# Kernel optimization log

Measured on AMD Instinct MI355X. Metric: run time of the kernel, lower is better.

Reference implementation:

```python
import jax, jax.numpy as jnp
import numpy as np

N_HEAD = 16
HEAD_DIM = 64
R_VALUE = 256
EPS_LN = 1e-5


def _orf(x, omega, b):
    # orthogonal random features: sqrt(2/r) * cos(x @ omega.T + b)
    r = b.shape[0]
    return jnp.sqrt(2.0 / r) * jnp.cos(x @ omega.T + b)


def _layernorm(x, gamma, beta):
    m = jnp.mean(x, axis=-1, keepdims=True)
    v = jnp.var(x, axis=-1, keepdims=True)
    return (x - m) / jnp.sqrt(v + EPS_LN) * gamma + beta


def setup_inputs() -> dict:
    key = jax.random.key(0)
    ks = jax.random.split(key, 12)
    B, L = 4, 2048
    dm = N_HEAD * HEAD_DIM  # 1024
    inp = {}
    inp["pre_query"] = jax.random.normal(ks[0], (B, L, dm), jnp.float32)
    inp["pre_key"] = jax.random.normal(ks[1], (B, L, dm), jnp.float32)
    inp["pre_value"] = jax.random.normal(ks[2], (B, L, dm), jnp.float32)
    inp["wq"] = jax.random.normal(ks[3], (dm, dm), jnp.float32) * 0.02
    inp["wk"] = jax.random.normal(ks[4], (dm, dm), jnp.float32) * 0.02
    inp["wv"] = jax.random.normal(ks[5], (dm, dm), jnp.float32) * 0.02
    inp["wo"] = jax.random.normal(ks[6], (dm, dm), jnp.float32) * 0.02
    inp["gamma"] = jnp.ones((dm,), jnp.float32)
    inp["beta"] = jnp.zeros((dm,), jnp.float32)
    G = jax.random.normal(ks[7], (R_VALUE, HEAD_DIM), jnp.float32)
    omega, _ = jnp.linalg.qr(G)  # (r, head_dim), orthonormal columns
    inp["omega"] = omega
    inp["b"] = jax.random.uniform(ks[8], (R_VALUE,), jnp.float32) * 2.0 * jnp.pi
    return inp


def reference(pre_query, pre_key, pre_value, wq, wk, wv, wo, gamma, beta, omega, b):
    B, L, dm = pre_query.shape
    H, D = N_HEAD, dm // N_HEAD
    q = (pre_query @ wq.T).reshape(B, L, H, D)
    k = (pre_key @ wk.T).reshape(B, L, H, D)
    v = (pre_value @ wv.T).reshape(B, L, H, D)

    qp = _orf(q, omega, b)  # (B,L,H,R)
    kp = _orf(k, omega, b)  # (B,L,H,R)

    # causal Performer attention as a linear-attention recurrence:
    # S_t = S_{t-1} + k'_t v_t^T ; z_t = z_{t-1} + k'_t
    # out_t = (q'_t . S_t) / clamp(q'_t . z_t)
    R = b.shape[0]
    S0 = jnp.zeros((B, H, R, D), qp.dtype)
    z0 = jnp.zeros((B, H, R), qp.dtype)

    def step(carry, xs):
        S, z = carry
        q_t, k_t, v_t = xs  # (B,H,R),(B,H,R),(B,H,D)
        S = S + k_t[..., :, None] * v_t[..., None, :]
        z = z + k_t
        num = jnp.einsum('bhr,bhrd->bhd', q_t, S)
        den = jnp.clip(jnp.einsum('bhr,bhr->bh', q_t, z), 1e-6, None)
        return (S, z), num / (den[..., None] + 1e-6)

    xs = (qp.transpose(1, 0, 2, 3), kp.transpose(1, 0, 2, 3), v.transpose(1, 0, 2, 3))
    _, out = jax.lax.scan(step, (S0, z0), xs)  # (L,B,H,D)
    out = out.transpose(1, 0, 2, 3).reshape(B, L, dm)

    pre_result = out @ wo.T
    return _layernorm(pre_result + pre_query, gamma, beta)
```

## Files before the change

kernel.cpp:

```cpp
#include <hip/hip_runtime.h>
#include <hip/hip_bf16.h>


typedef float f4 __attribute__((ext_vector_type(4)));
typedef __attribute__((ext_vector_type(8))) short bf16x8;
typedef __attribute__((ext_vector_type(4))) float f32x4;
typedef unsigned short u16x4 __attribute__((ext_vector_type(4)));
typedef unsigned short u16x8 __attribute__((ext_vector_type(8)));

#define B_  4
#define L_  2048
#define H_  16
#define D_  64
#define DM_ 1024
#define R_  256
#define C_  64
#define NC_ (L_ / C_)
#define M_  (B_ * L_)
#define M2_ (M_ * H_)

static __device__ __forceinline__ unsigned short f2bu(float x) {
    __hip_bfloat16 h = __float2bfloat16(x);
    return *(unsigned short*)&h;
}
static __device__ __forceinline__ float bu2f(unsigned short u) {
    union { unsigned int i; float f; } c; c.i = ((unsigned int)u) << 16; return c.f;
}

typedef __attribute__((address_space(3))) void lds_void_t;
typedef __attribute__((address_space(1))) const void gvoid_t;
static __device__ __forceinline__ void gload16(const void* g, void* l) {
    __builtin_amdgcn_global_load_lds((gvoid_t*)g, (lds_void_t*)l, 16, 0, 0);
}

__launch_bounds__(256)
__global__ void cvt_bf16(const float* __restrict__ in, unsigned short* __restrict__ out, int n4) {
    int i = blockIdx.x * 256 + threadIdx.x;
    if (i < n4) {
        f4 v = *(const f4*)&in[(size_t)i * 4];
        ushort4 o;
        o.x = f2bu(v[0]); o.y = f2bu(v[1]); o.z = f2bu(v[2]); o.w = f2bu(v[3]);
        *(ushort4*)&out[(size_t)i * 4] = o;
    }
}

__launch_bounds__(256)
__global__ void cvt_bf16_x3(const float* __restrict__ i0, const float* __restrict__ i1,
                            const float* __restrict__ i2,
                            unsigned short* __restrict__ o0, unsigned short* __restrict__ o1,
                            unsigned short* __restrict__ o2, int n4) {
    const int z = blockIdx.z;
    const float* in = (z == 0) ? i0 : (z == 1) ? i1 : i2;
    unsigned short* out = (z == 0) ? o0 : (z == 1) ? o1 : o2;
    int i = blockIdx.x * 256 + threadIdx.x;
    if (i < n4) {
        f4 v = *(const f4*)&in[(size_t)i * 4];
        ushort4 o;
        o.x = f2bu(v[0]); o.y = f2bu(v[1]); o.z = f2bu(v[2]); o.w = f2bu(v[3]);
        *(ushort4*)&out[(size_t)i * 4] = o;
    }
}

__launch_bounds__(256)
__global__ void gemm_mfma_b3(const unsigned short* __restrict__ A0, const unsigned short* __restrict__ A1,
                             const unsigned short* __restrict__ A2,
                             const unsigned short* __restrict__ B0, const unsigned short* __restrict__ B1,
                             const unsigned short* __restrict__ B2,
                             unsigned short* __restrict__ C0, unsigned short* __restrict__ C1,
                             unsigned short* __restrict__ C2,
                             int M, int N, int K) {
    __shared__ unsigned short Asl[3][128 * 32];
    __shared__ unsigned short Bsl[3][128 * 32];
    const int z = blockIdx.z;
    const unsigned short* A  = (z == 0) ? A0 : (z == 1) ? A1 : A2;
    const unsigned short* Bw = (z == 0) ? B0 : (z == 1) ? B1 : B2;
    unsigned short*       Cb = (z == 0) ? C0 : (z == 1) ? C1 : C2;
    const int t = threadIdx.x;
    const int lane = t & 63, w = t >> 6;
    const int wr = w >> 1, wc = w & 1;
    const int nwg = gridDim.x * gridDim.y;
    const int bid = blockIdx.y * gridDim.x + blockIdx.x;
    const int cpx = nwg >> 3;
    const int swz = (bid & 7) * cpx + (bid >> 3);
    const int row0 = (swz / gridDim.x) * 128, col0 = (swz % gridDim.x) * 128;
    const int sr0 = t >> 2;
    const int ssw = (((t & 3) ^ ((t >> 3) & 3)) * 8);
    const int lg = lane >> 4, lr = lane & 15;
    const int aslot = (lg ^ ((lr >> 1) & 3)) * 8;

#define STAGE_B3(buf, kkk) do { \
        gload16(&A [(size_t)(row0 + sr0)      * K + (kkk) + ssw], &Asl[buf][t * 8]); \
        gload16(&A [(size_t)(row0 + sr0 + 64) * K + (kkk) + ssw], &Asl[buf][(t + 256) * 8]); \
        gload16(&Bw[(size_t)(col0 + sr0)      * K + (kkk) + ssw], &Bsl[buf][t * 8]); \
        gload16(&Bw[(size_t)(col0 + sr0 + 64) * K + (kkk) + ssw], &Bsl[buf][(t + 256) * 8]); \
    } while (0)
#define COMPUTE_B3(buf) do { \
        bf16x8 af[4], bfr[4]; \
        _Pragma("unroll") \
        for (int m = 0; m < 4; ++m) \
            af[m] = *(const bf16x8*)&Asl[buf][(wr * 64 + m * 16 + lr) * 32 + aslot]; \
        _Pragma("unroll") \
        for (int n = 0; n < 4; ++n) \
            bfr[n] = *(const bf16x8*)&Bsl[buf][(wc * 64 + n * 16 + lr) * 32 + aslot]; \
        _Pragma("unroll") \
        for (int m = 0; m < 4; ++m) \
            _Pragma("unroll") \
            for (int n = 0; n < 4; ++n) \
                acc[m][n] = __builtin_amdgcn_mfma_f32_16x16x32_bf16(af[m], bfr[n], acc[m][n], 0, 0, 0); \
    } while (0)

    f32x4 acc[4][4] = {};
    STAGE_B3(0, 0);
    STAGE_B3(1, 32);
    int cur = 0;
    for (int kk = 0; kk + 64 < K; kk += 32) {
        int nx = cur + 2; if (nx >= 3) nx -= 3;
        STAGE_B3(nx, kk + 64);
        asm volatile("s_waitcnt vmcnt(8)" ::: "memory");
        __builtin_amdgcn_sched_barrier(0);
        __builtin_amdgcn_s_barrier();
        COMPUTE_B3(cur);
        __builtin_amdgcn_s_barrier();
        cur = (cur == 2) ? 0 : cur + 1;
    }
    asm volatile("s_waitcnt vmcnt(4)" ::: "memory");
    __builtin_amdgcn_sched_barrier(0);
    __builtin_amdgcn_s_barrier();
    COMPUTE_B3(cur);
    __builtin_amdgcn_s_barrier();
    cur = (cur == 2) ? 0 : cur + 1;
    asm volatile("s_waitcnt vmcnt(0)" ::: "memory");
    __builtin_amdgcn_sched_barrier(0);
    __builtin_amdgcn_s_barrier();
    COMPUTE_B3(cur);
#undef STAGE_B3
#undef COMPUTE_B3
#pragma unroll
    for (int m = 0; m < 4; ++m)
#pragma unroll
        for (int n = 0; n < 4; ++n)
#pragma unroll
            for (int i = 0; i < 4; ++i) {
                int r  = row0 + wr * 64 + m * 16 + lg * 4 + i;
                int cc = col0 + wc * 64 + n * 16 + lr;
                Cb[(size_t)r * N + cc] = f2bu(acc[m][n][i]);
            }
}

__launch_bounds__(256)
__global__ void gemm_out(const unsigned short* __restrict__ A,
                         const unsigned short* __restrict__ Bw,
                         const float* __restrict__ resid,
                         float* __restrict__ Cf,
                         int M, int N, int K) {
    __shared__ unsigned short Asl[3][64 * 32];
    __shared__ unsigned short Bsl[3][128 * 32];
    const int t = threadIdx.x;
    const int lane = t & 63, w = t >> 6;
    const int nwg = gridDim.x * gridDim.y;
    const int bid = blockIdx.y * gridDim.x + blockIdx.x;
    const int cpx = nwg >> 3;
    const int swz = (bid & 7) * cpx + (bid >> 3);
    const int row0 = (swz / gridDim.x) * 64, col0 = (swz % gridDim.x) * 128;
    const int sr0 = t >> 2;
    const int ssw = (((t & 3) ^ ((t >> 3) & 3)) * 8);
    const int lg = lane >> 4, lr = lane & 15;
    const int aslot = (lg ^ ((lr >> 1) & 3)) * 8;

#define STAGE_O(buf, kkk) do { \
        gload16(&A [(size_t)(row0 + sr0)      * K + (kkk) + ssw], &Asl[buf][t * 8]); \
        gload16(&Bw[(size_t)(col0 + sr0)      * K + (kkk) + ssw], &Bsl[buf][t * 8]); \
        gload16(&Bw[(size_t)(col0 + sr0 + 64) * K + (kkk) + ssw], &Bsl[buf][(t + 256) * 8]); \
    } while (0)
#define COMPUTE_O(buf) do { \
        bf16x8 af[4], bfr[2]; \
        _Pragma("unroll") \
        for (int m = 0; m < 4; ++m) \
            af[m] = *(const bf16x8*)&Asl[buf][(m * 16 + lr) * 32 + aslot]; \
        _Pragma("unroll") \
        for (int n = 0; n < 2; ++n) \
            bfr[n] = *(const bf16x8*)&Bsl[buf][(w * 32 + n * 16 + lr) * 32 + aslot]; \
        _Pragma("unroll") \
        for (int m = 0; m < 4; ++m) \
            _Pragma("unroll") \
            for (int n = 0; n < 2; ++n) \
                acc[m][n] = __builtin_amdgcn_mfma_f32_16x16x32_bf16(af[m], bfr[n], acc[m][n], 0, 0, 0); \
    } while (0)

    f32x4 acc[4][2] = {};
    STAGE_O(0, 0);
    STAGE_O(1, 32);
    int cur = 0;
    for (int kk = 0; kk + 64 < K; kk += 32) {
        int nx = cur + 2; if (nx >= 3) nx -= 3;
        STAGE_O(nx, kk + 64);
        asm volatile("s_waitcnt vmcnt(6)" ::: "memory");
        __builtin_amdgcn_sched_barrier(0);
        __builtin_amdgcn_s_barrier();
        COMPUTE_O(cur);
        __builtin_amdgcn_s_barrier();
        cur = (cur == 2) ? 0 : cur + 1;
    }
    asm volatile("s_waitcnt vmcnt(3)" ::: "memory");
    __builtin_amdgcn_sched_barrier(0);
    __builtin_amdgcn_s_barrier();
    COMPUTE_O(cur);
    __builtin_amdgcn_s_barrier();
    cur = (cur == 2) ? 0 : cur + 1;
    asm volatile("s_waitcnt vmcnt(0)" ::: "memory");
    __builtin_amdgcn_sched_barrier(0);
    __builtin_amdgcn_s_barrier();
    COMPUTE_O(cur);
#undef STAGE_O
#undef COMPUTE_O
#pragma unroll
    for (int m = 0; m < 4; ++m)
#pragma unroll
        for (int n = 0; n < 2; ++n)
#pragma unroll
            for (int i = 0; i < 4; ++i) {
                int r  = row0 + m * 16 + lg * 4 + i;
                int cc = col0 + w * 32 + n * 16 + lr;
                size_t off = (size_t)r * N + cc;
                Cf[off] = acc[m][n][i] + resid[off];
            }
}

#define RS_STRIDE 272
__launch_bounds__(256)
__global__ void feat_mfma_b2(const unsigned short* __restrict__ X0, const unsigned short* __restrict__ X1,
                             const unsigned short* __restrict__ om,
                             const float* __restrict__ bvec,
                             unsigned short* __restrict__ O0, unsigned short* __restrict__ O1) {
    __shared__ unsigned short Xs[2 * 64 * 32];
    __shared__ unsigned short Pool[64 * RS_STRIDE];
    const int z = blockIdx.z;
    const unsigned short* X = z ? X1 : X0;
    unsigned short* out = z ? O1 : O0;
    const int t = threadIdx.x;
    const int lane = t & 63, w = t >> 6;
    const int lg = lane >> 4, lr = lane & 15;
    const int m0 = blockIdx.x * 64;
    const int aslot = (lg ^ ((lr >> 1) & 3)) * 8;

#pragma unroll
    for (int i = 0; i < 2; ++i) {
        int cch = i * 256 + t;
        int ks = cch >> 8, row = (cch >> 2) & 63;
        int sub = ((cch & 3) ^ ((cch >> 3) & 3)) * 8;
        gload16(&X[(size_t)(m0 + row) * 64 + ks * 32 + sub], &Xs[cch * 8]);
    }
#pragma unroll
    for (int i = 0; i < 8; ++i) {
        int cch = i * 256 + t;
        int ks = cch >> 10, r = (cch >> 2) & 255;
        int sub = ((cch & 3) ^ ((cch >> 3) & 3)) * 8;
        gload16(&om[(size_t)r * 64 + ks * 32 + sub], &Pool[cch * 8]);
    }
    __syncthreads();

    f32x4 acc[4][4] = {};
#pragma unroll
    for (int ks = 0; ks < 2; ++ks) {
        bf16x8 af[4], bfr[4];
#pragma unroll
        for (int m = 0; m < 4; ++m)
            af[m] = *(const bf16x8*)&Xs[ks * 2048 + (m * 16 + lr) * 32 + aslot];
#pragma unroll
        for (int n = 0; n < 4; ++n)
            bfr[n] = *(const bf16x8*)&Pool[ks * 8192 + (w * 64 + n * 16 + lr) * 32 + aslot];
#pragma unroll
        for (int m = 0; m < 4; ++m)
#pragma unroll
            for (int n = 0; n < 4; ++n)
                acc[m][n] = __builtin_amdgcn_mfma_f32_16x16x32_bf16(af[m], bfr[n], acc[m][n], 0, 0, 0);
    }
    __syncthreads();

    const float scale = 0.08838834764831845f;
#pragma unroll
    for (int n = 0; n < 4; ++n) {
        const int col = w * 64 + n * 16 + lr;
        const float bb = bvec[col];
#pragma unroll
        for (int m = 0; m < 4; ++m)
#pragma unroll
            for (int ii = 0; ii < 4; ++ii)
                Pool[(m * 16 + lg * 4 + ii) * RS_STRIDE + col] = f2bu(scale * __cosf(acc[m][n][ii] + bb));
    }
    __syncthreads();
#pragma unroll
    for (int i = 0; i < 8; ++i) {
        int cch = i * 256 + t;
        int row = cch >> 5, colc = (cch & 31) * 8;
        u16x8 vv = *(const u16x8*)&Pool[row * RS_STRIDE + colc];
        *(u16x8*)&out[(size_t)(m0 + row) * 256 + colc] = vv;
    }
}

__launch_bounds__(256)
__global__ void passA_mfma(const unsigned short* __restrict__ kp, const unsigned short* __restrict__ vb,
                           unsigned short* __restrict__ kvT, float* __restrict__ ksum) {
    __shared__ __align__(16) unsigned short KPt[256][72];
    __shared__ __align__(16) unsigned short Vt[64][72];
    const int c = blockIdx.x, h = blockIdx.y, bz = blockIdx.z;
    const int t = threadIdx.x;
    const int lane = t & 63, w = t >> 6;
    const int lg = lane >> 4, lr = lane & 15;
    const int l0 = c * C_;
    const int bh = bz * H_ + h;

    {
        const int l4 = (t & 15) * 4, rs = (t >> 4) * 16;
        u16x8 row[4][2];
#pragma unroll
        for (int i = 0; i < 4; ++i) {
            const unsigned short* src = &kp[((size_t)(bz * L_ + l0 + l4 + i) * H_ + h) * R_ + rs];
            row[i][0] = *(const u16x8*)src;
            row[i][1] = *(const u16x8*)(src + 8);
        }
#pragma unroll
        for (int q = 0; q < 16; ++q) {
            u16x4 pk = { row[0][q >> 3][q & 7], row[1][q >> 3][q & 7],
                         row[2][q >> 3][q & 7], row[3][q >> 3][q & 7] };
            *(u16x4*)&KPt[rs + q][l4] = pk;
        }
    }
    {
        const int d4 = (t & 15) * 4, ls = (t >> 4) * 4;
        u16x4 x[4];
#pragma unroll
        for (int i = 0; i < 4; ++i)
            x[i] = *(const u16x4*)&vb[(size_t)(bz * L_ + l0 + ls + i) * DM_ + h * 64 + d4];
#pragma unroll
        for (int q = 0; q < 4; ++q) {
            u16x4 pk = { x[0][q], x[1][q], x[2][q], x[3][q] };
            *(u16x4*)&Vt[d4 + q][ls] = pk;
        }
    }
    __syncthreads();

    f32x4 acc[4][4] = {};
#pragma unroll
    for (int ks = 0; ks < 2; ++ks) {
        bf16x8 af[4], bfr[4];
#pragma unroll
        for (int m = 0; m < 4; ++m)
            af[m] = *(const bf16x8*)&KPt[64 * w + 16 * m + lr][ks * 32 + lg * 8];
#pragma unroll
        for (int n = 0; n < 4; ++n)
            bfr[n] = *(const bf16x8*)&Vt[16 * n + lr][ks * 32 + lg * 8];
#pragma unroll
        for (int m = 0; m < 4; ++m)
#pragma unroll
            for (int n = 0; n < 4; ++n)
                acc[m][n] = __builtin_amdgcn_mfma_f32_16x16x32_bf16(af[m], bfr[n], acc[m][n], 0, 0, 0);
    }
    size_t sbase = ((size_t)(bh * NC_ + c)) * 64 * R_;
#pragma unroll
    for (int n = 0; n < 4; ++n)
#pragma unroll
        for (int m = 0; m < 4; ++m) {
            int d = 16 * n + lr;
            int r = 64 * w + 16 * m + lg * 4;
            u16x4 pk = { f2bu(acc[m][n][0]), f2bu(acc[m][n][1]),
                         f2bu(acc[m][n][2]), f2bu(acc[m][n][3]) };
            *(u16x4*)&kvT[sbase + (size_t)d * R_ + r] = pk;
        }
    {
        float s = 0.f;
#pragma unroll
        for (int j = 0; j < 8; ++j) {
            u16x8 vv = *(const u16x8*)&KPt[t][j * 8];
#pragma unroll
            for (int q = 0; q < 8; ++q) s += bu2f(vv[q]);
        }
        ksum[((size_t)(bh * NC_ + c)) * R_ + t] = s;
    }
}

__launch_bounds__(256)
__global__ void passB_chain(unsigned short* __restrict__ kvT, float* __restrict__ ksum) {
    const int bx = blockIdx.x, h = blockIdx.y, bz = blockIdx.z;
    const int t = threadIdx.x;
    const int bh = bz * H_ + h;
    const int idx = bx * 256 + t;
    const int d = idx >> 6;
    const int rg = (idx & 63) * 4;
    size_t base = ((size_t)bh * NC_ * 64 + d) * R_ + rg;
    const size_t cstride = (size_t)64 * R_;
    float run0 = 0.f, run1 = 0.f, run2 = 0.f, run3 = 0.f;
    for (int c = 0; c < NC_; ++c) {
        size_t ix = base + (size_t)c * cstride;
        u16x4 v = *(const u16x4*)&kvT[ix];
        u16x4 o = { f2bu(run0), f2bu(run1), f2bu(run2), f2bu(run3) };
        *(u16x4*)&kvT[ix] = o;
        run0 += bu2f(v[0]); run1 += bu2f(v[1]);
        run2 += bu2f(v[2]); run3 += bu2f(v[3]);
    }
    if (bx == 0) {
        float rz = 0.f;
        for (int c = 0; c < NC_; ++c) {
            size_t ix = ((size_t)bh * NC_ + c) * R_ + t;
            float tmp = ksum[ix];
            ksum[ix] = rz;
            rz += tmp;
        }
    }
}

__launch_bounds__(256)
__global__ void passC_mfma(const unsigned short* __restrict__ qp, const unsigned short* __restrict__ kp,
                           const unsigned short* __restrict__ vb, const unsigned short* __restrict__ kvT,
                           const float* __restrict__ zpref, unsigned short* __restrict__ attnb) {
    __shared__ __align__(16) unsigned short Sl[64 * 256];
    __shared__ __align__(16) unsigned short Vt[80][72];
    __shared__ __align__(16) unsigned short As[64][72];

    const int c = blockIdx.x, h = blockIdx.y, bz = blockIdx.z;
    const int t = threadIdx.x;
    const int lane = t & 63, w = t >> 6;
    const int lg = lane >> 4, lr = lane & 15;
    const int l0 = c * C_;
    const int bh = bz * H_ + h;
    const size_t sbase = ((size_t)(bh * NC_ + c)) * 64 * R_;
    const size_t zbase = ((size_t)(bh * NC_ + c)) * R_;

#pragma unroll
    for (int i = 0; i < 8; ++i) {
        int idx = i * 256 + t;
        int row = idx >> 5, s = idx & 31;
        gload16(&kvT[sbase + (size_t)row * R_ + ((s ^ (row & 7)) << 3)], &Sl[idx * 8]);
    }

    {
        const int d4 = (t & 15) * 4, ls = (t >> 4) * 4;
        u16x4 x[4];
#pragma unroll
        for (int i = 0; i < 4; ++i)
            x[i] = *(const u16x4*)&vb[(size_t)(bz * L_ + l0 + ls + i) * DM_ + h * 64 + d4];
#pragma unroll
        for (int q = 0; q < 4; ++q) {
            u16x4 pk = { x[0][q], x[1][q], x[2][q], x[3][q] };
            *(u16x4*)&Vt[d4 + q][ls] = pk;
        }
    }
    if (t < 16) {
        u16x4 ones = { 0x3F80, 0x3F80, 0x3F80, 0x3F80 };
        *(u16x4*)&Vt[64][t * 4] = ones;
    }

    const size_t qrow = ((size_t)(bz * L_ + l0 + 16 * w + lr) * H_ + h) * R_;
    bf16x8 aq[8];
#pragma unroll
    for (int ks = 0; ks < 8; ++ks) aq[ks] = *(const bf16x8*)&qp[qrow + ks * 32 + lg * 8];

    f32x4 sacc[4] = {};
#pragma unroll
    for (int half = 0; half < 2; ++half) {
        bf16x8 bk[4][4];
#pragma unroll
        for (int k2 = 0; k2 < 4; ++k2)
#pragma unroll
            for (int n = 0; n < 4; ++n)
                bk[k2][n] = *(const bf16x8*)&kp[((size_t)(bz * L_ + l0 + 16 * n + lr) * H_ + h) * R_
                                                + (half * 4 + k2) * 32 + lg * 8];
        __builtin_amdgcn_s_setprio(1);
#pragma unroll
        for (int k2 = 0; k2 < 4; ++k2)
#pragma unroll
            for (int n = 0; n < 4; ++n)
                sacc[n] = __builtin_amdgcn_mfma_f32_16x16x32_bf16(aq[half * 4 + k2], bk[k2][n], sacc[n], 0, 0, 0);
        __builtin_amdgcn_s_setprio(0);
    }
#pragma unroll
    for (int n = 0; n < 4; ++n)
#pragma unroll
        for (int ii = 0; ii < 4; ++ii) {
            int i_loc = 16 * w + lg * 4 + ii;
            int j_loc = 16 * n + lr;
            As[i_loc][j_loc] = (j_loc <= i_loc) ? f2bu(sacc[n][ii]) : (unsigned short)0;
        }

    u16x8 zu[8];
#pragma unroll
    for (int ks = 0; ks < 8; ++ks) {
        f4 z0 = *(const f4*)&zpref[zbase + ks * 32 + lg * 8];
        f4 z1 = *(const f4*)&zpref[zbase + ks * 32 + lg * 8 + 4];
        zu[ks] = u16x8{ f2bu(z0[0]), f2bu(z0[1]), f2bu(z0[2]), f2bu(z0[3]),
                        f2bu(z1[0]), f2bu(z1[1]), f2bu(z1[2]), f2bu(z1[3]) };
    }
    __syncthreads();

    f32x4 oacc[4] = {};
    f32x4 dacc = {};
    __builtin_amdgcn_s_setprio(1);
#pragma unroll
    for (int ks = 0; ks < 8; ++ks) {
#pragma unroll
        for (int n = 0; n < 4; ++n) {
            int row = 16 * n + lr;
            int slot = (ks * 4 + lg) ^ (lr & 7);
            bf16x8 bs = *(const bf16x8*)&Sl[row * 256 + slot * 8];
            oacc[n] = __builtin_amdgcn_mfma_f32_16x16x32_bf16(aq[ks], bs, oacc[n], 0, 0, 0);
        }
        dacc = __builtin_amdgcn_mfma_f32_16x16x32_bf16(aq[ks], *(bf16x8*)&zu[ks], dacc, 0, 0, 0);
    }

    f32x4 racc = {};
#pragma unroll
    for (int ks = 0; ks < 2; ++ks) {
        bf16x8 aa = *(const bf16x8*)&As[16 * w + lr][ks * 32 + lg * 8];
#pragma unroll
        for (int n = 0; n < 4; ++n) {
            bf16x8 bv = *(const bf16x8*)&Vt[16 * n + lr][ks * 32 + lg * 8];
            oacc[n] = __builtin_amdgcn_mfma_f32_16x16x32_bf16(aa, bv, oacc[n], 0, 0, 0);
        }
        bf16x8 b4 = *(const bf16x8*)&Vt[64 + lr][ks * 32 + lg * 8];
        racc = __builtin_amdgcn_mfma_f32_16x16x32_bf16(aa, b4, racc, 0, 0, 0);
    }
    __builtin_amdgcn_s_setprio(0);

#pragma unroll
    for (int ii = 0; ii < 4; ++ii) {
        float rs_ = __shfl(racc[ii], lane & 48, 64);
        float den = rs_ + dacc[ii];
        float inv = 1.f / (fmaxf(den, 1e-6f) + 1e-6f);
#pragma unroll
        for (int n = 0; n < 4; ++n)
            attnb[(size_t)(bz * L_ + l0 + 16 * w + lg * 4 + ii) * DM_ + h * 64 + 16 * n + lr] =
                f2bu(oacc[n][ii] * inv);
    }
}

__launch_bounds__(256)
__global__ void ln_kernel(float* __restrict__ io, const float* __restrict__ gamma,
                          const float* __restrict__ beta) {
    __shared__ float wsum[4], wsum2[4];
    const int row = blockIdx.x;
    const int t = threadIdx.x;
    f4 x = *(const f4*)&io[(size_t)row * DM_ + t * 4];
    float s  = x[0] + x[1] + x[2] + x[3];
    float s2 = x[0]*x[0] + x[1]*x[1] + x[2]*x[2] + x[3]*x[3];
#pragma unroll
    for (int o = 32; o > 0; o >>= 1) {
        s  += __shfl_down(s, o);
        s2 += __shfl_down(s2, o);
    }
    if ((t & 63) == 0) { wsum[t >> 6] = s; wsum2[t >> 6] = s2; }
    __syncthreads();
    s  = wsum[0]  + wsum[1]  + wsum[2]  + wsum[3];
    s2 = wsum2[0] + wsum2[1] + wsum2[2] + wsum2[3];
    const float m = s * (1.f / DM_);
    const float var = s2 * (1.f / DM_) - m * m;
    const float rstd = rsqrtf(var + 1e-5f);
    f4 g  = *(const f4*)&gamma[t * 4];
    f4 bb = *(const f4*)&beta[t * 4];
    f4 o = (x - m) * rstd * g + bb;
    *(f4*)&io[(size_t)row * DM_ + t * 4] = o;
}

extern "C" void kernel_launch(void* const* d_in, const int* in_sizes, int n_in,
                              void* d_out, int out_size, void* d_ws, size_t ws_size,
                              hipStream_t stream) {
    const float* pre_q = (const float*)d_in[0];
    const float* pre_k = (const float*)d_in[1];
    const float* pre_v = (const float*)d_in[2];
    const float* wq    = (const float*)d_in[3];
    const float* wk    = (const float*)d_in[4];
    const float* wv    = (const float*)d_in[5];
    const float* wo    = (const float*)d_in[6];
    const float* gamma = (const float*)d_in[7];
    const float* beta  = (const float*)d_in[8];
    const float* omega = (const float*)d_in[9];
    const float* bvec  = (const float*)d_in[10];

    const size_t NEED = 226ull << 20;
    if (ws_size < NEED) return;

    char* w = (char*)d_ws;
    unsigned short* qp    = (unsigned short*)(w);
    unsigned short* kp    = (unsigned short*)(w + (64ull << 20));
    unsigned short* kvT   = (unsigned short*)(w + (128ull << 20));
    unsigned short* vb    = (unsigned short*)(w + (192ull << 20));
    unsigned short* attnb = (unsigned short*)(w + (208ull << 20));
    float*          ksum  = (float*)(w + (224ull << 20));
    unsigned short* aq    = (unsigned short*)(w);
    unsigned short* ak    = (unsigned short*)(w + (16ull << 20));
    unsigned short* av    = (unsigned short*)(w + (32ull << 20));
    unsigned short* wq_bf = (unsigned short*)(w + (48ull << 20));
    unsigned short* wk_bf = (unsigned short*)(w + (50ull << 20));
    unsigned short* wv_bf = (unsigned short*)(w + (52ull << 20));
    unsigned short* qx    = (unsigned short*)(w + (128ull << 20));
    unsigned short* kx    = (unsigned short*)(w + (144ull << 20));
    unsigned short* om_bf = (unsigned short*)(w + (208ull << 20));
    unsigned short* wo_bf = (unsigned short*)(w + (64ull << 20));
    float*          outb  = (float*)d_out;

    const int n4_big = M_ * DM_ / 4;
    const int n4_w   = DM_ * DM_ / 4;
    const int n4_om  = R_ * D_ / 4;
    dim3 gg3(DM_ / 128, M_ / 128, 3);
    dim3 ggo(DM_ / 128, M_ / 64);

    cvt_bf16_x3<<<dim3((n4_big + 255) / 256, 1, 3), 256, 0, stream>>>(
        pre_q, pre_k, pre_v, aq, ak, av, n4_big);
    cvt_bf16_x3<<<dim3((n4_w + 255) / 256, 1, 3), 256, 0, stream>>>(
        wq, wk, wv, wq_bf, wk_bf, wv_bf, n4_w);
    cvt_bf16<<<(n4_om + 255) / 256, 256, 0, stream>>>(omega, om_bf, n4_om);

    gemm_mfma_b3<<<gg3, 256, 0, stream>>>(aq, ak, av, wq_bf, wk_bf, wv_bf,
                                          qx, kx, vb, M_, DM_, DM_);
    feat_mfma_b2<<<dim3(M2_ / 64, 1, 2), 256, 0, stream>>>(qx, kx, om_bf, bvec, qp, kp);

    passA_mfma<<<dim3(NC_, H_, B_), 256, 0, stream>>>(kp, vb, kvT, ksum);
    passB_chain<<<dim3(16, H_, B_), 256, 0, stream>>>(kvT, ksum);
    passC_mfma<<<dim3(NC_, H_, B_), 256, 0, stream>>>(qp, kp, vb, kvT, ksum, attnb);

    cvt_bf16<<<(n4_w + 255) / 256, 256, 0, stream>>>(wo, wo_bf, n4_w);
    gemm_out<<<ggo, 256, 0, stream>>>(attnb, wo_bf, pre_q, outb, M_, DM_, DM_);
    ln_kernel<<<M_, 256, 0, stream>>>(outb, gamma, beta);
}
```

Measured before the change: 293.2 us.

## Enlarge QKV projection GEMM tiles to 256x256 with 512 threads, double buffering

The batched Q/K/V projection GEMM moves from 128x128 tiles with 4 waves and a triple-buffered LDS pipeline to 256x256 tiles with 8 waves, each wave computing a 128x64 sub-tile. LDS staging drops to double buffering. MFMA sections are wrapped in s_setprio to favour the math waves. The goal is more operand reuse per global and LDS load and fewer blocks. The cost is a smaller grid (384 blocks against 256 CUs, so uneven wave quantization), a shallower prefetch pipeline, and twice the accumulator registers per thread, which may lower occupancy.

```diff
diff --git a/kernel.cpp b/kernel.cpp
--- a/kernel.cpp
+++ b/kernel.cpp
@@ -61,7 +61,7 @@
     }
 }
 
-__launch_bounds__(256)
+__launch_bounds__(512)
 __global__ void gemm_mfma_b3(const unsigned short* __restrict__ A0, const unsigned short* __restrict__ A1,
                              const unsigned short* __restrict__ A2,
                              const unsigned short* __restrict__ B0, const unsigned short* __restrict__ B1,
@@ -69,79 +69,69 @@
                              unsigned short* __restrict__ C0, unsigned short* __restrict__ C1,
                              unsigned short* __restrict__ C2,
                              int M, int N, int K) {
-    __shared__ unsigned short Asl[3][128 * 32];
-    __shared__ unsigned short Bsl[3][128 * 32];
+    __shared__ unsigned short Asl[2][256 * 32];
+    __shared__ unsigned short Bsl[2][256 * 32];
     const int z = blockIdx.z;
     const unsigned short* A  = (z == 0) ? A0 : (z == 1) ? A1 : A2;
     const unsigned short* Bw = (z == 0) ? B0 : (z == 1) ? B1 : B2;
     unsigned short*       Cb = (z == 0) ? C0 : (z == 1) ? C1 : C2;
     const int t = threadIdx.x;
     const int lane = t & 63, w = t >> 6;
-    const int wr = w >> 1, wc = w & 1;
+    const int wr = w >> 2, wc = w & 3;
     const int nwg = gridDim.x * gridDim.y;
     const int bid = blockIdx.y * gridDim.x + blockIdx.x;
     const int cpx = nwg >> 3;
     const int swz = (bid & 7) * cpx + (bid >> 3);
-    const int row0 = (swz / gridDim.x) * 128, col0 = (swz % gridDim.x) * 128;
+    const int row0 = (swz / gridDim.x) * 256, col0 = (swz % gridDim.x) * 256;
     const int sr0 = t >> 2;
     const int ssw = (((t & 3) ^ ((t >> 3) & 3)) * 8);
     const int lg = lane >> 4, lr = lane & 15;
     const int aslot = (lg ^ ((lr >> 1) & 3)) * 8;
 
 #define STAGE_B3(buf, kkk) do { \
-        gload16(&A [(size_t)(row0 + sr0)      * K + (kkk) + ssw], &Asl[buf][t * 8]); \
-        gload16(&A [(size_t)(row0 + sr0 + 64) * K + (kkk) + ssw], &Asl[buf][(t + 256) * 8]); \
-        gload16(&Bw[(size_t)(col0 + sr0)      * K + (kkk) + ssw], &Bsl[buf][t * 8]); \
-        gload16(&Bw[(size_t)(col0 + sr0 + 64) * K + (kkk) + ssw], &Bsl[buf][(t + 256) * 8]); \
+        gload16(&A [(size_t)(row0 + sr0)       * K + (kkk) + ssw], &Asl[buf][t * 8]); \
+        gload16(&A [(size_t)(row0 + sr0 + 128) * K + (kkk) + ssw], &Asl[buf][(t + 512) * 8]); \
+        gload16(&Bw[(size_t)(col0 + sr0)       * K + (kkk) + ssw], &Bsl[buf][t * 8]); \
+        gload16(&Bw[(size_t)(col0 + sr0 + 128) * K + (kkk) + ssw], &Bsl[buf][(t + 512) * 8]); \
     } while (0)
-#define COMPUTE_B3(buf) do { \
-        bf16x8 af[4], bfr[4]; \
-        _Pragma("unroll") \
-        for (int m = 0; m < 4; ++m) \
-            af[m] = *(const bf16x8*)&Asl[buf][(wr * 64 + m * 16 + lr) * 32 + aslot]; \
-        _Pragma("unroll") \
-        for (int n = 0; n < 4; ++n) \
-            bfr[n] = *(const bf16x8*)&Bsl[buf][(wc * 64 + n * 16 + lr) * 32 + aslot]; \
-        _Pragma("unroll") \
-        for (int m = 0; m < 4; ++m) \
-            _Pragma("unroll") \
-            for (int n = 0; n < 4; ++n) \
-                acc[m][n] = __builtin_amdgcn_mfma_f32_16x16x32_bf16(af[m], bfr[n], acc[m][n], 0, 0, 0); \
-    } while (0)
-
-    f32x4 acc[4][4] = {};
+
+    f32x4 acc[8][4] = {};
     STAGE_B3(0, 0);
-    STAGE_B3(1, 32);
     int cur = 0;
-    for (int kk = 0; kk + 64 < K; kk += 32) {
-        int nx = cur + 2; if (nx >= 3) nx -= 3;
-        STAGE_B3(nx, kk + 64);
-        asm volatile("s_waitcnt vmcnt(8)" ::: "memory");
+    for (int kk = 0; kk < K; kk += 32) {
+        if (kk + 32 < K) {
+            STAGE_B3(cur ^ 1, kk + 32);
+            asm volatile("s_waitcnt vmcnt(4)" ::: "memory");
+        } else {
+            asm volatile("s_waitcnt vmcnt(0)" ::: "memory");
+        }
         __builtin_amdgcn_sched_barrier(0);
         __builtin_amdgcn_s_barrier();
-        COMPUTE_B3(cur);
+        bf16x8 af[8], bfr[4];
+#pragma unroll
+        for (int m = 0; m < 8; ++m)
+            af[m] = *(const bf16x8*)&Asl[cur][(wr * 128 + m * 16 + lr) * 32 + aslot];
+#pragma unroll
+        for (int n = 0; n < 4; ++n)
+            bfr[n] = *(const bf16x8*)&Bsl[cur][(wc * 64 + n * 16 + lr) * 32 + aslot];
+        __builtin_amdgcn_s_setprio(1);
+#pragma unroll
+        for (int m = 0; m < 8; ++m)
+#pragma unroll
+            for (int n = 0; n < 4; ++n)
+                acc[m][n] = __builtin_amdgcn_mfma_f32_16x16x32_bf16(af[m], bfr[n], acc[m][n], 0, 0, 0);
+        __builtin_amdgcn_s_setprio(0);
         __builtin_amdgcn_s_barrier();
-        cur = (cur == 2) ? 0 : cur + 1;
-    }
-    asm volatile("s_waitcnt vmcnt(4)" ::: "memory");
-    __builtin_amdgcn_sched_barrier(0);
-    __builtin_amdgcn_s_barrier();
-    COMPUTE_B3(cur);
-    __builtin_amdgcn_s_barrier();
-    cur = (cur == 2) ? 0 : cur + 1;
-    asm volatile("s_waitcnt vmcnt(0)" ::: "memory");
-    __builtin_amdgcn_sched_barrier(0);
-    __builtin_amdgcn_s_barrier();
-    COMPUTE_B3(cur);
+        cur ^= 1;
+    }
 #undef STAGE_B3
-#undef COMPUTE_B3
-#pragma unroll
-    for (int m = 0; m < 4; ++m)
+#pragma unroll
+    for (int m = 0; m < 8; ++m)
 #pragma unroll
         for (int n = 0; n < 4; ++n)
 #pragma unroll
             for (int i = 0; i < 4; ++i) {
-                int r  = row0 + wr * 64 + m * 16 + lg * 4 + i;
+                int r  = row0 + wr * 128 + m * 16 + lg * 4 + i;
                 int cc = col0 + wc * 64 + n * 16 + lr;
                 Cb[(size_t)r * N + cc] = f2bu(acc[m][n][i]);
             }
@@ -600,7 +590,7 @@
     const int n4_big = M_ * DM_ / 4;
     const int n4_w   = DM_ * DM_ / 4;
     const int n4_om  = R_ * D_ / 4;
-    dim3 gg3(DM_ / 128, M_ / 128, 3);
+    dim3 gg3(DM_ / 256, M_ / 256, 3);
     dim3 ggo(DM_ / 128, M_ / 64);
 
     cvt_bf16_x3<<<dim3((n4_big + 255) / 256, 1, 3), 256, 0, stream>>>(
@@ -609,7 +599,7 @@
         wq, wk, wv, wq_bf, wk_bf, wv_bf, n4_w);
     cvt_bf16<<<(n4_om + 255) / 256, 256, 0, stream>>>(omega, om_bf, n4_om);
 
-    gemm_mfma_b3<<<gg3, 256, 0, stream>>>(aq, ak, av, wq_bf, wk_bf, wv_bf,
+    gemm_mfma_b3<<<gg3, 512, 0, stream>>>(aq, ak, av, wq_bf, wk_bf, wv_bf,
                                           qx, kx, vb, M_, DM_, DM_);
     feat_mfma_b2<<<dim3(M2_ / 64, 1, 2), 256, 0, stream>>>(qx, kx, om_bf, bvec, qp, kp);
 
```

After: 316.8 us. 1.08x slower.
